# Optimization experiments

Measured on AMD Instinct MI355X. Metric: run time of the kernel, lower is better.

Reference implementation:

```python
import jax, jax.numpy as jnp
import numpy as np

B, S, D_IN, D_H = 8, 4096, 256, 512
EPS = 1e-6


def setup_inputs() -> dict:
    key = jax.random.key(0)
    ks = jax.random.split(key, 5)
    scale = 1.0 / np.sqrt(D_IN)  # torch Linear default init scale (uniform bound)
    x = jax.random.normal(ks[0], (B, S, D_IN), dtype=jnp.float32)
    Wi = jax.random.normal(ks[1], (D_IN, D_H), dtype=jnp.float32) * scale
    Wf = jax.random.normal(ks[2], (D_IN, D_H), dtype=jnp.float32) * scale
    Wo = jax.random.normal(ks[3], (D_IN, D_H), dtype=jnp.float32) * scale
    Wz = jax.random.normal(ks[4], (D_IN, D_H), dtype=jnp.float32) * scale
    zb = jnp.zeros((D_H,), dtype=jnp.float32)
    return {"x": x, "Wi": Wi, "bi": zb, "Wf": Wf, "bf": zb,
            "Wo": Wo, "bo": zb, "Wz": Wz, "bz": zb}


def _xlstm_forward(x, Wi, bi, Wf, bf, Wo, bo, Wz, bz):
    # Batched projections over all timesteps at once: [B,S,D_H] each.
    i_t = jnp.exp(jnp.clip(jnp.einsum('bsd,dh->bsh', x, Wi) + bi, -20.0, 0.0))
    f_t = jnp.exp(jnp.clip(jnp.einsum('bsd,dh->bsh', x, Wf) + bf, -20.0, 0.0))
    o_t = jax.nn.sigmoid(jnp.einsum('bsd,dh->bsh', x, Wo) + bo)
    z_t = jnp.tanh(jnp.einsum('bsd,dh->bsh', x, Wz) + bz)

    def step(carry, gates):
        c, n = carry
        i, f, o, z = gates
        c = f * c + i * z
        n = f * n + i
        h = o * (c / (n + EPS))
        return (c, n), h

    c0 = jnp.zeros((x.shape[0], Wi.shape[1]), dtype=x.dtype)
    n0 = jnp.ones((x.shape[0], Wi.shape[1]), dtype=x.dtype)
    # time-major scan over the recurrence
    gates_tm = tuple(jnp.swapaxes(g, 0, 1) for g in (i_t, f_t, o_t, z_t))  # [S,B,H]
    _, h_tm = jax.lax.scan(step, (c0, n0), gates_tm)
    return jnp.swapaxes(h_tm, 0, 1)  # [B,S,H]


def reference(x, Wi, bi, Wf, bf, Wo, bo, Wz, bz):
    return _xlstm_forward(x, Wi, bi, Wf, bf, Wo, bo, Wz, bz)
```

## Files before the change

### kernel.cpp

```cpp
#include <hip/hip_runtime.h>
#include <hip/hip_bf16.h>
#include <cstdint>
#include <cstddef>

typedef __hip_bfloat16 bf16;
typedef __attribute__((ext_vector_type(8))) short short8;
typedef __attribute__((ext_vector_type(4))) short short4v;
typedef __attribute__((ext_vector_type(4))) float floatx4;

#define BB 8
#define SS 4096
#define DIN 256
#define DH 512
#define NCH 256
#define CHUNK 16

__device__ __forceinline__ float sh2f(short v) {
    unsigned int u = ((unsigned int)(unsigned short)v) << 16;
    float f; __builtin_memcpy(&f, &u, 4); return f;
}
__device__ __forceinline__ float frcp(float x) { return __builtin_amdgcn_rcpf(x); }
__device__ __forceinline__ short f2sh(float a) {
    bf16 bv = __float2bfloat16(a);
    short sv; __builtin_memcpy(&sv, &bv, 2); return sv;
}

__global__ __launch_bounds__(256) void prep(
    const float* __restrict__ Wi, const float* __restrict__ Wf,
    const float* __restrict__ Wo, const float* __restrict__ Wz,
    bf16* __restrict__ Wt,
    const float* __restrict__ X, bf16* __restrict__ Xb, int tblk)
{
    const int bx = blockIdx.x;
    const int tid = threadIdx.x;
    if (bx < tblk) {
        int o = bx * 256 + tid;
        int r = o >> 8;
        int k = o & 255;
        int y = r >> 7;
        int c = r & 127;
        int g = c >> 5;
        int h = y * 32 + (c & 31);
        const float* W = (g == 0) ? Wi : (g == 1) ? Wf : (g == 2) ? Wo : Wz;
        Wt[o] = __float2bfloat16(W[(size_t)k * DH + h]);
    } else {
        const int idx = (bx - tblk) * 256 + tid;
        float4 v = ((const float4*)X)[idx];
        bf16 o4[4] = {__float2bfloat16(v.x), __float2bfloat16(v.y),
                      __float2bfloat16(v.z), __float2bfloat16(v.w)};
        ((short4v*)Xb)[idx] = *(const short4v*)o4;
    }
}

__device__ __forceinline__ void load16_lds(const bf16* g, short* l)
{
    __builtin_amdgcn_global_load_lds(
        (const __attribute__((address_space(1))) unsigned int*)g,
        (__attribute__((address_space(3))) unsigned int*)l,
        16, 0, 0);
}

__global__ __launch_bounds__(256) void gemm_mfma(
    const bf16* __restrict__ Xb, const bf16* __restrict__ Wt,
    const float* __restrict__ bi, const float* __restrict__ bfv,
    const float* __restrict__ bo, const float* __restrict__ bz,
    bf16* __restrict__ Pi, bf16* __restrict__ Pf,
    bf16* __restrict__ Po, bf16* __restrict__ Pz,
    float* __restrict__ Aa, float* __restrict__ Bca, float* __restrict__ Bna,
    int nb)
{
    __shared__ __align__(16) short smem[128 * 132];

    const int cpx = gridDim.x >> 3;
    const int logical = ((int)blockIdx.x & 7) * cpx + ((int)blockIdx.x >> 3);
    const int y  = logical & 15;
    const int m0 = (logical >> 4) * 128;
    const int n0 = y * 128;

    const int tid  = threadIdx.x;
    const int wave = tid >> 6, lane = tid & 63;
    const int wm   = (wave >> 1) * 64, wn = (wave & 1) * 64;
    const int l15  = lane & 15;
    const int q    = lane >> 4;

    floatx4 acc[4][4];
#pragma unroll
    for (int i = 0; i < 4; i++)
#pragma unroll
        for (int j = 0; j < 4; j++) acc[i][j] = (floatx4){0.f, 0.f, 0.f, 0.f};

    const int r_ld = tid >> 2;
    const int c_ld = tid & 3;
    const bf16* agp0 = Xb + (size_t)(m0 + r_ld) * DIN + c_ld * 8;
    const bf16* agp1 = Xb + (size_t)(m0 + 64 + r_ld) * DIN + c_ld * 8;
    const bf16* bgp0 = Wt + (size_t)(n0 + r_ld) * DIN + c_ld * 8;
    const bf16* bgp1 = Wt + (size_t)(n0 + 64 + r_ld) * DIN + c_ld * 8;

#define STAGE(K0, BUF)                                            \
    do {                                                          \
        short* A_ = smem + (BUF) * 8192;                          \
        short* B_ = A_ + 4096;                                    \
        load16_lds(agp0 + (K0), &A_[tid * 8]);                    \
        load16_lds(agp1 + (K0), &A_[2048 + tid * 8]);             \
        load16_lds(bgp0 + (K0), &B_[tid * 8]);                    \
        load16_lds(bgp1 + (K0), &B_[2048 + tid * 8]);             \
    } while (0)

    STAGE(0, 0);

#pragma unroll
    for (int k = 0; k < 8; k++) {
        const int cur = k & 1;
        if (k < 7) STAGE((k + 1) * 32, cur ^ 1);
        if (k < 7) asm volatile("s_waitcnt vmcnt(4)" ::: "memory");
        else       asm volatile("s_waitcnt vmcnt(0)" ::: "memory");
        __builtin_amdgcn_s_barrier();

        const short* A = smem + cur * 8192;
        const short* B = A + 4096;
        short8 af[4], bfr[4];
#pragma unroll
        for (int ti = 0; ti < 4; ti++)
            af[ti] = *(const short8*)&A[(wm + ti * 16 + l15) * 32 + q * 8];
#pragma unroll
        for (int tj = 0; tj < 4; tj++)
            bfr[tj] = *(const short8*)&B[(wn + tj * 16 + l15) * 32 + q * 8];
#pragma unroll
        for (int ti = 0; ti < 4; ti++)
#pragma unroll
            for (int tj = 0; tj < 4; tj++)
                acc[ti][tj] = __builtin_amdgcn_mfma_f32_16x16x32_bf16(
                    af[ti], bfr[tj], acc[ti][tj], 0, 0, 0);
        asm volatile("s_waitcnt lgkmcnt(0)" ::: "memory");
        __builtin_amdgcn_s_barrier();
    }
#undef STAGE

#pragma unroll
    for (int ti = 0; ti < 4; ti++) {
        const int mrow = wm + ti * 16 + q * 4;
#pragma unroll
        for (int tj = 0; tj < 4; tj++) {
            const int cb = wn + tj * 16;
            const int g  = cb >> 5;
            const int c  = cb + l15;
            const float* bp = (g == 0) ? bi : (g == 1) ? bfv
                            : (g == 2) ? bo : bz;
            const float bsv = bp[y * 32 + (c & 31)];
#pragma unroll
            for (int r = 0; r < 4; r++) {
                const float v = acc[ti][tj][r] + bsv;
                float a;
                if (g == 0 || g == 1) {
                    a = __expf(fminf(fmaxf(v, -20.f), 0.f));
                } else if (g == 2) {
                    a = frcp(1.f + __expf(-v));
                } else {
                    a = 1.f - 2.f * frcp(__expf(2.f * v) + 1.f);
                }
                smem[(mrow + r) * 132 + c] = f2sh(a);
            }
        }
    }
    __syncthreads();

    const int bidx = m0 / SS;

    {
        const int cp  = (tid & 31) * 4;
        const int g2  = cp >> 5;
        const int hb  = y * 32 + (cp & 31);
        bf16* pl = ((g2 == 0) ? Pi : (g2 == 1) ? Pf : (g2 == 2) ? Po : Pz) + hb;
        const int r0 = tid >> 5;
#pragma unroll
        for (int t = 0; t < 16; t++) {
            const int row = t * 8 + r0;
            short4v v = *(const short4v*)&smem[row * 132 + cp];
            *(short4v*)(pl + (size_t)(m0 + row) * DH) = v;
        }
    }

    {
        const int hh = tid & 31;
        const int ch = tid >> 5;
        float A = 1.f, Bc = 0.f, Bn = 0.f;
        const short* base = &smem[(ch * CHUNK) * 132];
#pragma unroll
        for (int s = 0; s < CHUNK; s++) {
            const short* rp = base + s * 132;
            const float iv = sh2f(rp[hh]);
            const float f  = sh2f(rp[32 + hh]);
            const float zv = sh2f(rp[96 + hh]);
            Bc = fmaf(f, Bc, iv * zv);
            Bn = fmaf(f, Bn, iv);
            A *= f;
        }
        const int ch_g = ((m0 % SS) >> 4) + ch;
        const int hgl  = y * 32 + hh;
        const size_t cidx = (size_t)(ch_g * nb + bidx) * DH + hgl;
        Aa[cidx] = A; Bca[cidx] = Bc; Bna[cidx] = Bn;
    }
}

__global__ __launch_bounds__(256) void scan_chunks(
    float* __restrict__ Aa, float* __restrict__ Bca,
    const float* __restrict__ Bna, int nb)
{
    __shared__ float sA[4][64], sBc[4][64], sBn[4][64];
    const int tid = threadIdx.x;
    const int t   = blockIdx.x * 64 + (tid & 63);
    const int s   = tid >> 6;
    const int stride = nb * DH;
    const int SEG = NCH / 4;

    float A = 1.f, Bc = 0.f, Bn = 0.f;
    for (int k = 0; k < SEG; k++) {
        const size_t cidx = (size_t)(s * SEG + k) * stride + t;
        const float a  = Aa[cidx];
        const float bc = Bca[cidx];
        const float bn = Bna[cidx];
        Bc = fmaf(a, Bc, bc);
        Bn = fmaf(a, Bn, bn);
        A *= a;
    }
    sA[s][tid & 63] = A; sBc[s][tid & 63] = Bc; sBn[s][tid & 63] = Bn;
    __syncthreads();

    float c = 0.f, n = 1.f;
#pragma unroll
    for (int s2 = 0; s2 < 3; s2++) {
        if (s2 < s) {
            const float a  = sA[s2][tid & 63];
            const float nc = fmaf(a, c, sBc[s2][tid & 63]);
            n = fmaf(a, n, sBn[s2][tid & 63]);
            c = nc;
        }
    }

    for (int k = 0; k < SEG; k++) {
        const size_t cidx = (size_t)(s * SEG + k) * stride + t;
        const float a  = Aa[cidx];
        const float bc = Bca[cidx];
        const float bn = Bna[cidx];
        Aa[cidx] = c; Bca[cidx] = n;
        const float nc = fmaf(a, c, bc);
        n = fmaf(a, n, bn);
        c = nc;
    }
}

__global__ __launch_bounds__(256) void scan_emit(
    const bf16* __restrict__ Pi, const bf16* __restrict__ Pf,
    const bf16* __restrict__ Po, const bf16* __restrict__ Pz,
    const float* __restrict__ Cs, const float* __restrict__ Ns,
    float* __restrict__ out, int nb)
{
    const int tid = threadIdx.x;
    const int ch  = blockIdx.x * 2 + (tid >> 7);
    const int b   = blockIdx.y;
    const int hg  = (tid & 127) * 4;
    const size_t base = ((size_t)(b * SS + ch * CHUNK)) * DH + hg;
    const size_t cidx = (size_t)(ch * nb + b) * DH + hg;

    float c[4], n[4];
    *(floatx4*)c = *(const floatx4*)(Cs + cidx);
    *(floatx4*)n = *(const floatx4*)(Ns + cidx);

#pragma unroll 4
    for (int s = 0; s < CHUNK; s++) {
        const size_t o = base + (size_t)s * DH;
        short4v i4 = *(const short4v*)(Pi + o);
        short4v f4 = *(const short4v*)(Pf + o);
        short4v o4 = *(const short4v*)(Po + o);
        short4v z4 = *(const short4v*)(Pz + o);
        float h[4];
#pragma unroll
        for (int j = 0; j < 4; j++) {
            const float f  = sh2f(f4[j]);
            const float iv = sh2f(i4[j]);
            const float ov = sh2f(o4[j]);
            const float zv = sh2f(z4[j]);
            c[j] = fmaf(f, c[j], iv * zv);
            n[j] = fmaf(f, n[j], iv);
            h[j] = ov * c[j] * frcp(n[j] + 1e-6f);
        }
        *(floatx4*)(out + o) = *(floatx4*)h;
    }
}

extern "C" void kernel_launch(void* const* d_in, const int* in_sizes, int n_in,
                              void* d_out, int out_size, void* d_ws, size_t ws_size,
                              hipStream_t stream)
{
    const float* x   = (const float*)d_in[0];
    const float* Wi  = (const float*)d_in[1];
    const float* bi  = (const float*)d_in[2];
    const float* Wf  = (const float*)d_in[3];
    const float* bfv = (const float*)d_in[4];
    const float* Wo  = (const float*)d_in[5];
    const float* bo  = (const float*)d_in[6];
    const float* Wz  = (const float*)d_in[7];
    const float* bz  = (const float*)d_in[8];
    float* out = (float*)d_out;

    int nb = BB;
    while (nb > 1) {
        size_t need = (1u << 20)
                    + (size_t)nb * SS * DIN * 2
                    + 4 * (size_t)nb * SS * DH * 2
                    + 3 * (size_t)NCH * nb * DH * 4;
        if (need <= ws_size) break;
        nb >>= 1;
    }

    const size_t plane = (size_t)nb * SS * DH;
    bf16* Wt = (bf16*)d_ws;
    bf16* Xb = (bf16*)((char*)d_ws + (1u << 20));
    bf16* Pi = Xb + (size_t)nb * SS * DIN;
    bf16* Pf = Pi + plane;
    bf16* Po = Pf + plane;
    bf16* Pz = Po + plane;
    float* Aa  = (float*)(Pz + plane);
    float* Bca = Aa  + (size_t)NCH * nb * DH;
    float* Bna = Bca + (size_t)NCH * nb * DH;

    for (int b0 = 0; b0 < BB; b0 += nb) {
        const float* Xsrc = x   + (size_t)b0 * SS * DIN;
        float*       Ob   = out + (size_t)b0 * SS * DH;
        const int tblk = (b0 == 0) ? 2048 : 0;
        prep<<<tblk + nb * 1024, 256, 0, stream>>>(
            Wi, Wf, Wo, Wz, Wt, Xsrc, Xb, tblk);
        gemm_mfma<<<nb * 512, 256, 0, stream>>>(
            Xb, Wt, bi, bfv, bo, bz, Pi, Pf, Po, Pz, Aa, Bca, Bna, nb);
        scan_chunks<<<nb * 8, 256, 0, stream>>>(Aa, Bca, Bna, nb);
        scan_emit<<<dim3(NCH / 2, nb), 256, 0, stream>>>(
            Pi, Pf, Po, Pz, Aa, Bca, Ob, nb);
    }
}
```

Before: 228.4 us.

## Fuse fp32-to-bf16 X conversion into GEMM and merge chunk scan via last-block counter

```diff
diff --git a/kernel.cpp b/kernel.cpp
--- a/kernel.cpp
+++ b/kernel.cpp
@@ -28,12 +28,11 @@
 __global__ __launch_bounds__(256) void prep(
     const float* __restrict__ Wi, const float* __restrict__ Wf,
     const float* __restrict__ Wo, const float* __restrict__ Wz,
-    bf16* __restrict__ Wt,
-    const float* __restrict__ X, bf16* __restrict__ Xb, int tblk)
+    bf16* __restrict__ Wt, unsigned int* __restrict__ Ctr)
 {
     const int bx = blockIdx.x;
     const int tid = threadIdx.x;
-    if (bx < tblk) {
+    if (bx < 2048) {
         int o = bx * 256 + tid;
         int r = o >> 8;
         int k = o & 255;
@@ -44,11 +43,7 @@
         const float* W = (g == 0) ? Wi : (g == 1) ? Wf : (g == 2) ? Wo : Wz;
         Wt[o] = __float2bfloat16(W[(size_t)k * DH + h]);
     } else {
-        const int idx = (bx - tblk) * 256 + tid;
-        float4 v = ((const float4*)X)[idx];
-        bf16 o4[4] = {__float2bfloat16(v.x), __float2bfloat16(v.y),
-                      __float2bfloat16(v.z), __float2bfloat16(v.w)};
-        ((short4v*)Xb)[idx] = *(const short4v*)o4;
+        if (tid < 8) Ctr[tid] = 0u;
     }
 }
 
@@ -60,16 +55,17 @@
         16, 0, 0);
 }
 
-__global__ __launch_bounds__(256) void gemm_mfma(
-    const bf16* __restrict__ Xb, const bf16* __restrict__ Wt,
+__global__ __launch_bounds__(256) void gemm_scan(
+    const float* __restrict__ X, const bf16* __restrict__ Wt,
     const float* __restrict__ bi, const float* __restrict__ bfv,
     const float* __restrict__ bo, const float* __restrict__ bz,
     bf16* __restrict__ Pi, bf16* __restrict__ Pf,
     bf16* __restrict__ Po, bf16* __restrict__ Pz,
     float* __restrict__ Aa, float* __restrict__ Bca, float* __restrict__ Bna,
-    int nb)
+    unsigned int* __restrict__ Ctr, int nb, int pass)
 {
     __shared__ __align__(16) short smem[128 * 132];
+    __shared__ int s_rank;
 
     const int cpx = gridDim.x >> 3;
     const int logical = ((int)blockIdx.x & 7) * cpx + ((int)blockIdx.x >> 3);
@@ -91,50 +87,85 @@
 
     const int r_ld = tid >> 2;
     const int c_ld = tid & 3;
-    const bf16* agp0 = Xb + (size_t)(m0 + r_ld) * DIN + c_ld * 8;
-    const bf16* agp1 = Xb + (size_t)(m0 + 64 + r_ld) * DIN + c_ld * 8;
+    const float* xg0 = X + (size_t)(m0 + r_ld) * DIN + c_ld * 8;
+    const float* xg1 = xg0 + (size_t)64 * DIN;
     const bf16* bgp0 = Wt + (size_t)(n0 + r_ld) * DIN + c_ld * 8;
     const bf16* bgp1 = Wt + (size_t)(n0 + 64 + r_ld) * DIN + c_ld * 8;
 
-#define STAGE(K0, BUF)                                            \
-    do {                                                          \
-        short* A_ = smem + (BUF) * 8192;                          \
-        short* B_ = A_ + 4096;                                    \
-        load16_lds(agp0 + (K0), &A_[tid * 8]);                    \
-        load16_lds(agp1 + (K0), &A_[2048 + tid * 8]);             \
-        load16_lds(bgp0 + (K0), &B_[tid * 8]);                    \
-        load16_lds(bgp1 + (K0), &B_[2048 + tid * 8]);             \
+    float4 a00, a01, a10, a11;
+#define ISSUE_A(K0)                                                   \
+    do {                                                              \
+        a00 = *(const float4*)(xg0 + (K0));                           \
+        a01 = *(const float4*)(xg0 + (K0) + 4);                       \
+        a10 = *(const float4*)(xg1 + (K0));                           \
+        a11 = *(const float4*)(xg1 + (K0) + 4);                       \
     } while (0)
-
-    STAGE(0, 0);
+#define ISSUE_B(K0, Bb)                                               \
+    do {                                                              \
+        load16_lds(bgp0 + (K0), &(Bb)[tid * 8]);                      \
+        load16_lds(bgp1 + (K0), &(Bb)[2048 + tid * 8]);               \
+    } while (0)
+#define WRITE_A(Ab)                                                   \
+    do {                                                              \
+        bf16 t0[8] = {__float2bfloat16(a00.x), __float2bfloat16(a00.y), \
+                      __float2bfloat16(a00.z), __float2bfloat16(a00.w), \
+                      __float2bfloat16(a01.x), __float2bfloat16(a01.y), \
+                      __float2bfloat16(a01.z), __float2bfloat16(a01.w)};\
+        *(short8*)&(Ab)[tid * 8] = *(const short8*)t0;                \
+        bf16 t1[8] = {__float2bfloat16(a10.x), __float2bfloat16(a10.y), \
+                      __float2bfloat16(a10.z), __float2bfloat16(a10.w), \
+                      __float2bfloat16(a11.x), __float2bfloat16(a11.y), \
+                      __float2bfloat16(a11.z), __float2bfloat16(a11.w)};\
+        *(short8*)&(Ab)[2048 + tid * 8] = *(const short8*)t1;         \
+    } while (0)
+
+    ISSUE_A(0);
+    ISSUE_B(0, smem + 4096);
+    asm volatile("s_waitcnt vmcnt(2)" ::: "memory");
+    WRITE_A(smem);
+    asm volatile("s_waitcnt lgkmcnt(0)" ::: "memory");
+    __builtin_amdgcn_s_barrier();
 
 #pragma unroll
     for (int k = 0; k < 8; k++) {
         const int cur = k & 1;
-        if (k < 7) STAGE((k + 1) * 32, cur ^ 1);
-        if (k < 7) asm volatile("s_waitcnt vmcnt(4)" ::: "memory");
-        else       asm volatile("s_waitcnt vmcnt(0)" ::: "memory");
+        short* Ab = smem + cur * 8192;
+        short* Bb = Ab + 4096;
+        short* An = smem + (cur ^ 1) * 8192;
+        short* Bn = An + 4096;
+        if (k < 7) {
+            ISSUE_A((k + 1) * 32);
+            ISSUE_B((k + 1) * 32, Bn);
+            asm volatile("s_waitcnt vmcnt(6)" ::: "memory");
+        } else {
+            asm volatile("s_waitcnt vmcnt(0)" ::: "memory");
+        }
         __builtin_amdgcn_s_barrier();
 
-        const short* A = smem + cur * 8192;
-        const short* B = A + 4096;
         short8 af[4], bfr[4];
 #pragma unroll
         for (int ti = 0; ti < 4; ti++)
-            af[ti] = *(const short8*)&A[(wm + ti * 16 + l15) * 32 + q * 8];
+            af[ti] = *(const short8*)&Ab[(wm + ti * 16 + l15) * 32 + q * 8];
 #pragma unroll
         for (int tj = 0; tj < 4; tj++)
-            bfr[tj] = *(const short8*)&B[(wn + tj * 16 + l15) * 32 + q * 8];
+            bfr[tj] = *(const short8*)&Bb[(wn + tj * 16 + l15) * 32 + q * 8];
 #pragma unroll
         for (int ti = 0; ti < 4; ti++)
 #pragma unroll
             for (int tj = 0; tj < 4; tj++)
                 acc[ti][tj] = __builtin_amdgcn_mfma_f32_16x16x32_bf16(
                     af[ti], bfr[tj], acc[ti][tj], 0, 0, 0);
+
+        if (k < 7) {
+            asm volatile("s_waitcnt vmcnt(2)" ::: "memory");
+            WRITE_A(An);
+        }
         asm volatile("s_waitcnt lgkmcnt(0)" ::: "memory");
         __builtin_amdgcn_s_barrier();
     }
-#undef STAGE
+#undef ISSUE_A
+#undef ISSUE_B
+#undef WRITE_A
 
 #pragma unroll
     for (int ti = 0; ti < 4; ti++) {
@@ -200,52 +231,69 @@
         const size_t cidx = (size_t)(ch_g * nb + bidx) * DH + hgl;
         Aa[cidx] = A; Bca[cidx] = Bc; Bna[cidx] = Bn;
     }
-}
-
-__global__ __launch_bounds__(256) void scan_chunks(
-    float* __restrict__ Aa, float* __restrict__ Bca,
-    const float* __restrict__ Bna, int nb)
-{
-    __shared__ float sA[4][64], sBc[4][64], sBn[4][64];
-    const int tid = threadIdx.x;
-    const int t   = blockIdx.x * 64 + (tid & 63);
-    const int s   = tid >> 6;
-    const int stride = nb * DH;
-    const int SEG = NCH / 4;
-
-    float A = 1.f, Bc = 0.f, Bn = 0.f;
-    for (int k = 0; k < SEG; k++) {
-        const size_t cidx = (size_t)(s * SEG + k) * stride + t;
-        const float a  = Aa[cidx];
-        const float bc = Bca[cidx];
-        const float bn = Bna[cidx];
-        Bc = fmaf(a, Bc, bc);
-        Bn = fmaf(a, Bn, bn);
-        A *= a;
-    }
-    sA[s][tid & 63] = A; sBc[s][tid & 63] = Bc; sBn[s][tid & 63] = Bn;
+
     __syncthreads();
-
-    float c = 0.f, n = 1.f;
-#pragma unroll
-    for (int s2 = 0; s2 < 3; s2++) {
-        if (s2 < s) {
-            const float a  = sA[s2][tid & 63];
-            const float nc = fmaf(a, c, sBc[s2][tid & 63]);
-            n = fmaf(a, n, sBn[s2][tid & 63]);
+    if (tid == 0) {
+        __threadfence();
+        unsigned int old = __hip_atomic_fetch_add(
+            &Ctr[pass], 1u, __ATOMIC_RELAXED, __HIP_MEMORY_SCOPE_AGENT);
+        s_rank = (int)old - (int)(gridDim.x - nb * 8);
+    }
+    __syncthreads();
+    const int rank = s_rank;
+    if (rank < 0) return;
+
+    if (tid == 0) {
+        while (__hip_atomic_load(&Ctr[pass], __ATOMIC_RELAXED,
+                                 __HIP_MEMORY_SCOPE_AGENT) < gridDim.x)
+            __builtin_amdgcn_s_sleep(32);
+    }
+    __syncthreads();
+    __threadfence();
+
+    {
+        float* sA  = (float*)smem;
+        float* sBc = sA + 256;
+        float* sBn = sBc + 256;
+        const int l  = tid & 63;
+        const int t  = rank * 64 + l;
+        const int s  = tid >> 6;
+        const int stride = nb * DH;
+        const int SEG = NCH / 4;
+
+        float A = 1.f, Bc = 0.f, Bn = 0.f;
+        for (int k = 0; k < SEG; k++) {
+            const size_t cidx = (size_t)(s * SEG + k) * stride + t;
+            const float a  = Aa[cidx];
+            const float bc = Bca[cidx];
+            const float bn = Bna[cidx];
+            Bc = fmaf(a, Bc, bc);
+            Bn = fmaf(a, Bn, bn);
+            A *= a;
+        }
+        sA[s * 64 + l] = A; sBc[s * 64 + l] = Bc; sBn[s * 64 + l] = Bn;
+        __syncthreads();
+
+        float c = 0.f, n = 1.f;
+#pragma unroll
+        for (int s2 = 0; s2 < 3; s2++) {
+            if (s2 < s) {
+                const float a  = sA[s2 * 64 + l];
+                const float nc = fmaf(a, c, sBc[s2 * 64 + l]);
+                n = fmaf(a, n, sBn[s2 * 64 + l]);
+                c = nc;
+            }
+        }
+        for (int k = 0; k < SEG; k++) {
+            const size_t cidx = (size_t)(s * SEG + k) * stride + t;
+            const float a  = Aa[cidx];
+            const float bc = Bca[cidx];
+            const float bn = Bna[cidx];
+            Aa[cidx] = c; Bca[cidx] = n;
+            const float nc = fmaf(a, c, bc);
+            n = fmaf(a, n, bn);
             c = nc;
         }
-    }
-
-    for (int k = 0; k < SEG; k++) {
-        const size_t cidx = (size_t)(s * SEG + k) * stride + t;
-        const float a  = Aa[cidx];
-        const float bc = Bca[cidx];
-        const float bn = Bna[cidx];
-        Aa[cidx] = c; Bca[cidx] = n;
-        const float nc = fmaf(a, c, bc);
-        n = fmaf(a, n, bn);
-        c = nc;
     }
 }
 
@@ -306,33 +354,33 @@
     int nb = BB;
     while (nb > 1) {
         size_t need = (1u << 20)
-                    + (size_t)nb * SS * DIN * 2
                     + 4 * (size_t)nb * SS * DH * 2
-                    + 3 * (size_t)NCH * nb * DH * 4;
+                    + 3 * (size_t)NCH * nb * DH * 4
+                    + 64;
         if (need <= ws_size) break;
         nb >>= 1;
     }
 
     const size_t plane = (size_t)nb * SS * DH;
     bf16* Wt = (bf16*)d_ws;
-    bf16* Xb = (bf16*)((char*)d_ws + (1u << 20));
-    bf16* Pi = Xb + (size_t)nb * SS * DIN;
+    bf16* Pi = (bf16*)((char*)d_ws + (1u << 20));
     bf16* Pf = Pi + plane;
     bf16* Po = Pf + plane;
     bf16* Pz = Po + plane;
     float* Aa  = (float*)(Pz + plane);
     float* Bca = Aa  + (size_t)NCH * nb * DH;
     float* Bna = Bca + (size_t)NCH * nb * DH;
-
-    for (int b0 = 0; b0 < BB; b0 += nb) {
+    unsigned int* Ctr = (unsigned int*)(Bna + (size_t)NCH * nb * DH);
+
+    prep<<<2049, 256, 0, stream>>>(Wi, Wf, Wo, Wz, Wt, Ctr);
+
+    int pass = 0;
+    for (int b0 = 0; b0 < BB; b0 += nb, pass++) {
         const float* Xsrc = x   + (size_t)b0 * SS * DIN;
         float*       Ob   = out + (size_t)b0 * SS * DH;
-        const int tblk = (b0 == 0) ? 2048 : 0;
-        prep<<<tblk + nb * 1024, 256, 0, stream>>>(
-            Wi, Wf, Wo, Wz, Wt, Xsrc, Xb, tblk);
-        gemm_mfma<<<nb * 512, 256, 0, stream>>>(
-            Xb, Wt, bi, bfv, bo, bz, Pi, Pf, Po, Pz, Aa, Bca, Bna, nb);
-        scan_chunks<<<nb * 8, 256, 0, stream>>>(Aa, Bca, Bna, nb);
+        gemm_scan<<<nb * 512, 256, 0, stream>>>(
+            Xsrc, Wt, bi, bfv, bo, bz, Pi, Pf, Po, Pz,
+            Aa, Bca, Bna, Ctr, nb, pass);
         scan_emit<<<dim3(NCH / 2, nb), 256, 0, stream>>>(
             Pi, Pf, Po, Pz, Aa, Bca, Ob, nb);
     }
```

After: 428.8 us. 87.8% more time.
